# Kernel tuning notes

Hardware: AMD Instinct MI355X
Metric: run time of the kernel (lower is better)

## Reference

```python
import jax, jax.numpy as jnp
import numpy as np


def setup_inputs() -> dict:
    key = jax.random.key(0)
    k1, k2, k3, k4, k5 = jax.random.split(key, 5)
    b, c, k, h, w = 8, 512, 19, 128, 128
    x = jax.random.normal(k1, (b, c, h, w), dtype=jnp.float32)
    # mask_conv: 1x1 conv ichn->ochn (weight [k, c], bias [k])
    Wm = jax.random.normal(k2, (k, c), dtype=jnp.float32) * (1.0 / np.sqrt(c))
    bm = jax.random.normal(k3, (k,), dtype=jnp.float32) * 0.02
    # filter_conv: grouped 1x1 conv, groups=k -> per-class [c_out, c_in] matmul
    Wf = jax.random.normal(k4, (k, c, c), dtype=jnp.float32) * (1.0 / np.sqrt(c))
    bf = jax.random.normal(k5, (k, c), dtype=jnp.float32) * 0.02
    return {"x": x, "Wm": Wm, "bm": bm, "Wf": Wf, "bf": bf}


def reference(x, Wm, bm, Wf, bf):
    b, c, h, w = x.shape
    k = Wm.shape[0]
    # mask_conv (1x1) + sigmoid -> [b, k, h, w]
    pre_mask = jnp.einsum('bchw,kc->bkhw', x, Wm) + bm[None, :, None, None]
    mask = jax.nn.sigmoid(pre_mask)
    # masked pooling: bmm(mask [b,k,hw], feat [b,hw,c]) / (h*w) -> [b, k, c]
    class_feat = jnp.einsum('bkhw,bchw->bkc', mask, x) / (h * w)
    # grouped 1x1 filter_conv: per class k, [c_out, c_in] GEMM on class_feat
    filters = jnp.einsum('koc,bkc->bko', Wf, class_feat) + bf[None, :, :]  # [b, k, c]
    # per-sample dynamic 1x1 conv (groups=b) == batched GEMM over channels
    pred = jnp.einsum('bkc,bchw->bkhw', filters, x)
    return pred
```

## Files before the change

### kernel.cpp

```cpp
#include <hip/hip_runtime.h>
#include <math.h>

#define BB 8
#define CC 512
#define KK 19
#define HWHW 16384
#define INV_HW (1.0f/16384.0f)

typedef __attribute__((ext_vector_type(8))) short bf16x8;
typedef __attribute__((ext_vector_type(4))) short s16x4;
typedef __attribute__((ext_vector_type(4))) float f32x4;

__device__ __forceinline__ unsigned short f2bf(float f) {
    unsigned int u = __float_as_uint(f);
    u = (u + 0x7fffu + ((u >> 16) & 1u)) >> 16;
    return (unsigned short)u;
}

__device__ __forceinline__ unsigned int pk_bf16(float a, float b) {
    unsigned int r;
    asm("v_cvt_pk_bf16_f32 %0, %1, %2" : "=v"(r) : "v"(a), "v"(b));
    return r;
}

__global__ __launch_bounds__(256, 3) void k_s1(const float* __restrict__ x,
                                               const float* __restrict__ Wm,
                                               const float* __restrict__ bm,
                                               unsigned short* __restrict__ mask) {
    __shared__ short wm[20 * CC];
    __shared__ short xt[2][128 * 64];
    const int tid = threadIdx.x;
    const int b = blockIdx.x >> 7;
    const int p0 = (blockIdx.x & 127) << 7;
    const float* xb = x + ((size_t)b * CC) * HWHW + p0;

    for (int u = tid; u < 20 * 128; u += 256) {
        const int k = u >> 7;
        const int c4 = (u & 127) << 2;
        float4 w = {0.f, 0.f, 0.f, 0.f};
        if (k < KK) w = *(const float4*)(Wm + k * CC + c4);
        s16x4 v = { (short)f2bf(w.x), (short)f2bf(w.y), (short)f2bf(w.z), (short)f2bf(w.w) };
        *(s16x4*)&wm[(k << 9) + (((c4 >> 3) ^ (k & 7)) << 3) + (c4 & 7)] = v;
    }

    const int wv = tid >> 6, ln = tid & 63;
    const int lm = ln & 15, q = ln >> 4;
    const f32x4 zz = {0.f, 0.f, 0.f, 0.f};
    f32x4 acc[2][2];
    acc[0][0] = zz; acc[0][1] = zz; acc[1][0] = zz; acc[1][1] = zz;

    const int cg0 = tid >> 5;
    const int pA  = (tid & 31) << 2;
    const float* sA = xb + (size_t)(cg0 << 2) * HWHW + pA;
    const float* sB = xb + (size_t)((cg0 + 8) << 2) * HWHW + pA;

    float4 Fa[8], Fb[8];
#pragma unroll
    for (int j = 0; j < 4; ++j) {
        Fa[j]     = *(const float4*)(sA + (size_t)j * HWHW);
        Fa[4 + j] = *(const float4*)(sB + (size_t)j * HWHW);
    }

#pragma unroll
    for (int cs = 0; cs < 8; ++cs) {
        const float4* cur = (cs & 1) ? Fb : Fa;
        float4* nxt = (cs & 1) ? Fa : Fb;
        if (cs < 7) {
            const size_t co = (size_t)((cs + 1) << 6) * HWHW;
#pragma unroll
            for (int j = 0; j < 4; ++j) {
                nxt[j]     = *(const float4*)(sA + co + (size_t)j * HWHW);
                nxt[4 + j] = *(const float4*)(sB + co + (size_t)j * HWHW);
            }
        }
        short* xts = (short*)xt[cs & 1];
#pragma unroll
        for (int h = 0; h < 2; ++h) {
            const int cg = cg0 + (h << 3);
            const float* G0 = (const float*)&cur[(h << 2) + 0];
            const float* G1 = (const float*)&cur[(h << 2) + 1];
            const float* G2 = (const float*)&cur[(h << 2) + 2];
            const float* G3 = (const float*)&cur[(h << 2) + 3];
#pragma unroll
            for (int j = 0; j < 4; ++j) {
                const int pr = pA + j;
                uint2 v = make_uint2(pk_bf16(G0[j], G1[j]), pk_bf16(G2[j], G3[j]));
                *(uint2*)&xts[(pr << 6) + (((cg >> 1) ^ (pr & 7)) << 3) + ((cg & 1) << 2)] = v;
            }
        }
        asm volatile("s_waitcnt lgkmcnt(0)" ::: "memory");
        __builtin_amdgcn_s_barrier();
        asm volatile("" ::: "memory");
#pragma unroll
        for (int ks = 0; ks < 2; ++ks) {
            const int gch = (cs << 3) + (ks << 2) + q;
            const int m1 = (lm < 3) ? (16 + lm) : 19;
            bf16x8 a0 = *(const bf16x8*)&wm[(lm << 9) + ((gch ^ (lm & 7)) << 3)];
            bf16x8 a1 = *(const bf16x8*)&wm[(m1 << 9) + ((gch ^ (m1 & 7)) << 3)];
            const int lch = (ks << 2) + q;
#pragma unroll
            for (int nt = 0; nt < 2; ++nt) {
                const int pr = (((wv << 1) + nt) << 4) + lm;
                bf16x8 bv = *(const bf16x8*)&xts[(pr << 6) + ((lch ^ (pr & 7)) << 3)];
                acc[0][nt] = __builtin_amdgcn_mfma_f32_16x16x32_bf16(a0, bv, acc[0][nt], 0, 0, 0);
                acc[1][nt] = __builtin_amdgcn_mfma_f32_16x16x32_bf16(a1, bv, acc[1][nt], 0, 0, 0);
            }
        }
    }

    unsigned short* mb = mask + ((size_t)b * KK) * HWHW + p0;
#pragma unroll
    for (int mt = 0; mt < 2; ++mt)
#pragma unroll
        for (int r = 0; r < 4; ++r) {
            const int k = (mt << 4) + (q << 2) + r;
            if (k < KK) {
                const float bias = bm[k];
#pragma unroll
                for (int nt = 0; nt < 2; ++nt) {
                    const int p = (((wv << 1) + nt) << 4) + lm;
                    const float t = acc[mt][nt][r] + bias;
                    mb[(size_t)k * HWHW + p] = f2bf(1.0f / (1.0f + __expf(-t)));
                }
            }
        }
}

__global__ __launch_bounds__(256, 4) void k_s2(const float* __restrict__ x,
                                               const unsigned short* __restrict__ mask,
                                               float* __restrict__ cf_part) {
    __shared__ short mt_[2][20 * 64];
    __shared__ short xtl[2][64 * 64];
    const int tid = threadIdx.x;
    const int s = blockIdx.x & 15;
    const int ct = (blockIdx.x >> 4) & 7;
    const int b = blockIdx.x >> 7;
    const int wv = tid >> 6, ln = tid & 63;
    const int lm = ln & 15, q = ln >> 4;
    const float* xb = x + ((size_t)b * CC + (ct << 6)) * HWHW + (s << 10);
    const unsigned short* mbs = mask + ((size_t)b * KK) * HWHW + (s << 10);

    const int mk = tid >> 3, mch = tid & 7;
    const int xc = tid >> 4;
    const int pq = tid & 15;

    const f32x4 zz = {0.f, 0.f, 0.f, 0.f};
    f32x4 acc[2];
    acc[0] = zz; acc[1] = zz;

    float4 Xa[4], Xb[4];
    uint4 Ma = make_uint4(0u,0u,0u,0u), Mb = make_uint4(0u,0u,0u,0u);

    if (tid < 160 && mk < KK) Ma = *(const uint4*)(mbs + (size_t)mk * HWHW + (mch << 3));
#pragma unroll
    for (int r = 0; r < 4; ++r)
        Xa[r] = *(const float4*)(xb + (size_t)(xc + (r << 4)) * HWHW + (pq << 2));

#pragma unroll
    for (int kp = 0; kp < 16; ++kp) {
        const float4* curX = (kp & 1) ? Xb : Xa;
        float4* nxtX = (kp & 1) ? Xa : Xb;
        const uint4 curM = (kp & 1) ? Mb : Ma;
        uint4* nxtM = (kp & 1) ? &Ma : &Mb;
        if (kp < 15) {
            if (tid < 160 && mk < KK)
                *nxtM = *(const uint4*)(mbs + (size_t)mk * HWHW + ((kp + 1) << 6) + (mch << 3));
#pragma unroll
            for (int r = 0; r < 4; ++r)
                nxtX[r] = *(const float4*)(xb + (size_t)(xc + (r << 4)) * HWHW + ((kp + 1) << 6) + (pq << 2));
        }
        short* mts = (short*)mt_[kp & 1];
        short* xls = (short*)xtl[kp & 1];
        if (tid < 160)
            *(uint4*)&mts[(mk << 6) + ((mch ^ (mk & 7)) << 3)] = curM;
#pragma unroll
        for (int r = 0; r < 4; ++r) {
            const int c = xc + (r << 4);
            const float* G = (const float*)&curX[r];
            uint2 v = make_uint2(pk_bf16(G[0], G[1]), pk_bf16(G[2], G[3]));
            *(uint2*)&xls[(c << 6) + (((pq >> 1) ^ (c & 7)) << 3) + ((pq & 1) << 2)] = v;
        }
        asm volatile("s_waitcnt lgkmcnt(0)" ::: "memory");
        __builtin_amdgcn_s_barrier();
        asm volatile("" ::: "memory");
#pragma unroll
        for (int ks = 0; ks < 2; ++ks) {
            const int pch = (ks << 2) + q;
            const int cr = (wv << 4) + lm;
            bf16x8 bv = *(const bf16x8*)&xls[(cr << 6) + ((pch ^ (cr & 7)) << 3)];
            const int m1 = (lm < 3) ? (16 + lm) : 19;
            bf16x8 a0 = *(const bf16x8*)&mts[(lm << 6) + ((pch ^ (lm & 7)) << 3)];
            bf16x8 a1 = *(const bf16x8*)&mts[(m1 << 6) + ((pch ^ (m1 & 7)) << 3)];
            acc[0] = __builtin_amdgcn_mfma_f32_16x16x32_bf16(a0, bv, acc[0], 0, 0, 0);
            acc[1] = __builtin_amdgcn_mfma_f32_16x16x32_bf16(a1, bv, acc[1], 0, 0, 0);
        }
    }

    float* dst = cf_part + ((size_t)(s * BB + b) * KK) * CC + (ct << 6) + (wv << 4) + lm;
#pragma unroll
    for (int mt = 0; mt < 2; ++mt)
#pragma unroll
        for (int r = 0; r < 4; ++r) {
            const int k = (mt << 4) + (q << 2) + r;
            if (k < KK) dst[(size_t)k * CC] = acc[mt][r];
        }
}

__global__ __launch_bounds__(256) void k_s2r(const float* __restrict__ part,
                                             float* __restrict__ cf) {
    const int i = blockIdx.x * 256 + threadIdx.x;
    if (i >= BB * KK * CC) return;
    const int b = i / (KK * CC);
    const int rem = i - b * (KK * CC);
    float sum = 0.0f;
#pragma unroll
    for (int s = 0; s < 16; ++s)
        sum += part[((size_t)(s * BB + b) * KK) * CC + rem];
    cf[i] = sum * INV_HW;
}

__global__ __launch_bounds__(256) void k_filters(const float* __restrict__ Wf,
                                                 const float* __restrict__ bf,
                                                 const float* __restrict__ cf,
                                                 float* __restrict__ fil) {
    const int blk = blockIdx.x;
    const int k = blk >> 7;
    const int o = ((blk & 127) << 2) + (threadIdx.x >> 6);
    const int lane = threadIdx.x & 63;
    const float* wrow = Wf + ((size_t)k * CC + o) * CC;

    float acc[BB];
#pragma unroll
    for (int b = 0; b < BB; ++b) acc[b] = 0.0f;
#pragma unroll
    for (int j = 0; j < CC / 64; ++j) {
        const int c = lane + (j << 6);
        const float wv = wrow[c];
#pragma unroll
        for (int b = 0; b < BB; ++b)
            acc[b] += wv * cf[((size_t)b * KK + k) * CC + c];
    }
#pragma unroll
    for (int b = 0; b < BB; ++b) {
#pragma unroll
        for (int off = 32; off > 0; off >>= 1)
            acc[b] += __shfl_down(acc[b], off, 64);
    }
    if (lane == 0) {
        const float bias = bf[k * CC + o];
#pragma unroll
        for (int b = 0; b < BB; ++b)
            fil[((size_t)b * KK + k) * CC + o] = acc[b] + bias;
    }
}

__global__ __launch_bounds__(256, 3) void k_s4(const float* __restrict__ x,
                                               const float* __restrict__ fil,
                                               float* __restrict__ out) {
    __shared__ short wm[20 * CC];
    __shared__ short xt[2][128 * 64];
    const int tid = threadIdx.x;
    const int b = blockIdx.x >> 7;
    const int p0 = (blockIdx.x & 127) << 7;
    const float* xb = x + ((size_t)b * CC) * HWHW + p0;
    const float* fb = fil + ((size_t)b * KK) * CC;

    for (int u = tid; u < 20 * 128; u += 256) {
        const int k = u >> 7;
        const int c4 = (u & 127) << 2;
        float4 w = {0.f, 0.f, 0.f, 0.f};
        if (k < KK) w = *(const float4*)(fb + k * CC + c4);
        s16x4 v = { (short)f2bf(w.x), (short)f2bf(w.y), (short)f2bf(w.z), (short)f2bf(w.w) };
        *(s16x4*)&wm[(k << 9) + (((c4 >> 3) ^ (k & 7)) << 3) + (c4 & 7)] = v;
    }

    const int wv = tid >> 6, ln = tid & 63;
    const int lm = ln & 15, q = ln >> 4;
    const f32x4 zz = {0.f, 0.f, 0.f, 0.f};
    f32x4 acc[2][2];
    acc[0][0] = zz; acc[0][1] = zz; acc[1][0] = zz; acc[1][1] = zz;

    const int cg0 = tid >> 5;
    const int pA  = (tid & 31) << 2;
    const float* sA = xb + (size_t)(cg0 << 2) * HWHW + pA;
    const float* sB = xb + (size_t)((cg0 + 8) << 2) * HWHW + pA;

    float4 Fa[8], Fb[8];
#pragma unroll
    for (int j = 0; j < 4; ++j) {
        Fa[j]     = *(const float4*)(sA + (size_t)j * HWHW);
        Fa[4 + j] = *(const float4*)(sB + (size_t)j * HWHW);
    }

#pragma unroll
    for (int cs = 0; cs < 8; ++cs) {
        const float4* cur = (cs & 1) ? Fb : Fa;
        float4* nxt = (cs & 1) ? Fa : Fb;
        if (cs < 7) {
            const size_t co = (size_t)((cs + 1) << 6) * HWHW;
#pragma unroll
            for (int j = 0; j < 4; ++j) {
                nxt[j]     = *(const float4*)(sA + co + (size_t)j * HWHW);
                nxt[4 + j] = *(const float4*)(sB + co + (size_t)j * HWHW);
            }
        }
        short* xts = (short*)xt[cs & 1];
#pragma unroll
        for (int h = 0; h < 2; ++h) {
            const int cg = cg0 + (h << 3);
            const float* G0 = (const float*)&cur[(h << 2) + 0];
            const float* G1 = (const float*)&cur[(h << 2) + 1];
            const float* G2 = (const float*)&cur[(h << 2) + 2];
            const float* G3 = (const float*)&cur[(h << 2) + 3];
#pragma unroll
            for (int j = 0; j < 4; ++j) {
                const int pr = pA + j;
                uint2 v = make_uint2(pk_bf16(G0[j], G1[j]), pk_bf16(G2[j], G3[j]));
                *(uint2*)&xts[(pr << 6) + (((cg >> 1) ^ (pr & 7)) << 3) + ((cg & 1) << 2)] = v;
            }
        }
        asm volatile("s_waitcnt lgkmcnt(0)" ::: "memory");
        __builtin_amdgcn_s_barrier();
        asm volatile("" ::: "memory");
#pragma unroll
        for (int ks = 0; ks < 2; ++ks) {
            const int gch = (cs << 3) + (ks << 2) + q;
            const int m1 = (lm < 3) ? (16 + lm) : 19;
            bf16x8 a0 = *(const bf16x8*)&wm[(lm << 9) + ((gch ^ (lm & 7)) << 3)];
            bf16x8 a1 = *(const bf16x8*)&wm[(m1 << 9) + ((gch ^ (m1 & 7)) << 3)];
            const int lch = (ks << 2) + q;
#pragma unroll
            for (int nt = 0; nt < 2; ++nt) {
                const int pr = (((wv << 1) + nt) << 4) + lm;
                bf16x8 bv = *(const bf16x8*)&xts[(pr << 6) + ((lch ^ (pr & 7)) << 3)];
                acc[0][nt] = __builtin_amdgcn_mfma_f32_16x16x32_bf16(a0, bv, acc[0][nt], 0, 0, 0);
                acc[1][nt] = __builtin_amdgcn_mfma_f32_16x16x32_bf16(a1, bv, acc[1][nt], 0, 0, 0);
            }
        }
    }

    float* ob = out + ((size_t)b * KK) * HWHW + p0;
#pragma unroll
    for (int mt = 0; mt < 2; ++mt)
#pragma unroll
        for (int r = 0; r < 4; ++r) {
            const int k = (mt << 4) + (q << 2) + r;
            if (k < KK) {
#pragma unroll
                for (int nt = 0; nt < 2; ++nt) {
                    const int p = (((wv << 1) + nt) << 4) + lm;
                    ob[(size_t)k * HWHW + p] = acc[mt][nt][r];
                }
            }
        }
}

extern "C" void kernel_launch(void* const* d_in, const int* in_sizes, int n_in,
                              void* d_out, int out_size, void* d_ws, size_t ws_size,
                              hipStream_t stream) {
    const float* x  = (const float*)d_in[0];
    const float* Wm = (const float*)d_in[1];
    const float* bm = (const float*)d_in[2];
    const float* Wf = (const float*)d_in[3];
    const float* bf = (const float*)d_in[4];
    float* out = (float*)d_out;

    unsigned short* mask = (unsigned short*)d_ws;
    float* cf_part = (float*)((char*)d_ws + (size_t)BB * KK * HWHW * 2);
    float* cf  = cf_part + (size_t)16 * BB * KK * CC;
    float* fil = cf + (size_t)BB * KK * CC;

    k_s1<<<1024, 256, 0, stream>>>(x, Wm, bm, mask);
    k_s2<<<1024, 256, 0, stream>>>(x, mask, cf_part);
    k_s2r<<<(BB * KK * CC + 255) / 256, 256, 0, stream>>>(cf_part, cf);
    k_filters<<<KK * 128, 256, 0, stream>>>(Wf, bf, cf, fil);
    k_s4<<<1024, 256, 0, stream>>>(x, fil, out);
}
```

Baseline: 470.3 us.

## Stage pre-swizzled bf16 copies of x in the first pass for reuse downstream

```diff
diff --git a/kernel.cpp b/kernel.cpp
--- a/kernel.cpp
+++ b/kernel.cpp
@@ -26,12 +26,15 @@
 __global__ __launch_bounds__(256, 3) void k_s1(const float* __restrict__ x,
                                                const float* __restrict__ Wm,
                                                const float* __restrict__ bm,
-                                               unsigned short* __restrict__ mask) {
+                                               unsigned short* __restrict__ mask,
+                                               unsigned short* __restrict__ xt4g,
+                                               unsigned short* __restrict__ xt2g) {
     __shared__ short wm[20 * CC];
     __shared__ short xt[2][128 * 64];
     const int tid = threadIdx.x;
     const int b = blockIdx.x >> 7;
-    const int p0 = (blockIdx.x & 127) << 7;
+    const int pt = blockIdx.x & 127;
+    const int p0 = pt << 7;
     const float* xb = x + ((size_t)b * CC) * HWHW + p0;
 
     for (int u = tid; u < 20 * 128; u += 256) {
@@ -51,8 +54,14 @@
 
     const int cg0 = tid >> 5;
     const int pA  = (tid & 31) << 2;
+    const int pqT = (tid & 31) & 15;
+    const int sS  = pt >> 3;
+    const int kpT = ((pt & 7) << 1) | ((tid & 31) >> 4);
     const float* sA = xb + (size_t)(cg0 << 2) * HWHW + pA;
     const float* sB = xb + (size_t)((cg0 + 8) << 2) * HWHW + pA;
+    unsigned short* t4fix = xt4g + ((size_t)((b << 7) | pt) << 16);
+    unsigned short* t2fix = xt2g + ((size_t)(b << 3) << 20)
+                                 + ((size_t)((sS << 4) | kpT) << 12);
 
     float4 Fa[8], Fb[8];
 #pragma unroll
@@ -74,6 +83,8 @@
             }
         }
         short* xts = (short*)xt[cs & 1];
+        unsigned short* t4 = t4fix + ((size_t)cs << 13);
+        unsigned short* t2 = t2fix + ((size_t)cs << 20);
 #pragma unroll
         for (int h = 0; h < 2; ++h) {
             const int cg = cg0 + (h << 3);
@@ -85,7 +96,17 @@
             for (int j = 0; j < 4; ++j) {
                 const int pr = pA + j;
                 uint2 v = make_uint2(pk_bf16(G0[j], G1[j]), pk_bf16(G2[j], G3[j]));
-                *(uint2*)&xts[(pr << 6) + (((cg >> 1) ^ (pr & 7)) << 3) + ((cg & 1) << 2)] = v;
+                const int idx = (pr << 6) + (((cg >> 1) ^ (pr & 7)) << 3) + ((cg & 1) << 2);
+                *(uint2*)&xts[idx] = v;
+                *(uint2*)&t4[idx] = v;
+            }
+#pragma unroll
+            for (int rr = 0; rr < 4; ++rr) {
+                const int cl = (cg << 2) + rr;
+                const float* Gr = (const float*)&cur[(h << 2) + rr];
+                uint2 w = make_uint2(pk_bf16(Gr[0], Gr[1]), pk_bf16(Gr[2], Gr[3]));
+                const int idx2 = (cl << 6) + (((pqT >> 1) ^ (cl & 7)) << 3) + ((pqT & 1) << 2);
+                *(uint2*)&t2[idx2] = w;
             }
         }
         asm volatile("s_waitcnt lgkmcnt(0)" ::: "memory");
@@ -126,7 +147,7 @@
         }
 }
 
-__global__ __launch_bounds__(256, 4) void k_s2(const float* __restrict__ x,
+__global__ __launch_bounds__(256, 4) void k_s2(const unsigned short* __restrict__ xt2g,
                                                const unsigned short* __restrict__ mask,
                                                float* __restrict__ cf_part) {
     __shared__ short mt_[2][20 * 64];
@@ -137,49 +158,40 @@
     const int b = blockIdx.x >> 7;
     const int wv = tid >> 6, ln = tid & 63;
     const int lm = ln & 15, q = ln >> 4;
-    const float* xb = x + ((size_t)b * CC + (ct << 6)) * HWHW + (s << 10);
     const unsigned short* mbs = mask + ((size_t)b * KK) * HWHW + (s << 10);
+    const unsigned short* tb = xt2g + ((size_t)((((b << 3) | ct) << 4) | s) << 16);
 
     const int mk = tid >> 3, mch = tid & 7;
-    const int xc = tid >> 4;
-    const int pq = tid & 15;
 
     const f32x4 zz = {0.f, 0.f, 0.f, 0.f};
     f32x4 acc[2];
     acc[0] = zz; acc[1] = zz;
 
-    float4 Xa[4], Xb[4];
+    uint4 Xa[2], Xb2[2];
     uint4 Ma = make_uint4(0u,0u,0u,0u), Mb = make_uint4(0u,0u,0u,0u);
 
     if (tid < 160 && mk < KK) Ma = *(const uint4*)(mbs + (size_t)mk * HWHW + (mch << 3));
-#pragma unroll
-    for (int r = 0; r < 4; ++r)
-        Xa[r] = *(const float4*)(xb + (size_t)(xc + (r << 4)) * HWHW + (pq << 2));
+    Xa[0] = *(const uint4*)(tb + (tid << 4));
+    Xa[1] = *(const uint4*)(tb + (tid << 4) + 8);
 
 #pragma unroll
     for (int kp = 0; kp < 16; ++kp) {
-        const float4* curX = (kp & 1) ? Xb : Xa;
-        float4* nxtX = (kp & 1) ? Xa : Xb;
+        const uint4* curX = (kp & 1) ? Xb2 : Xa;
+        uint4* nxtX = (kp & 1) ? Xa : Xb2;
         const uint4 curM = (kp & 1) ? Mb : Ma;
         uint4* nxtM = (kp & 1) ? &Ma : &Mb;
         if (kp < 15) {
             if (tid < 160 && mk < KK)
                 *nxtM = *(const uint4*)(mbs + (size_t)mk * HWHW + ((kp + 1) << 6) + (mch << 3));
-#pragma unroll
-            for (int r = 0; r < 4; ++r)
-                nxtX[r] = *(const float4*)(xb + (size_t)(xc + (r << 4)) * HWHW + ((kp + 1) << 6) + (pq << 2));
+            nxtX[0] = *(const uint4*)(tb + ((kp + 1) << 12) + (tid << 4));
+            nxtX[1] = *(const uint4*)(tb + ((kp + 1) << 12) + (tid << 4) + 8);
         }
         short* mts = (short*)mt_[kp & 1];
         short* xls = (short*)xtl[kp & 1];
         if (tid < 160)
             *(uint4*)&mts[(mk << 6) + ((mch ^ (mk & 7)) << 3)] = curM;
-#pragma unroll
-        for (int r = 0; r < 4; ++r) {
-            const int c = xc + (r << 4);
-            const float* G = (const float*)&curX[r];
-            uint2 v = make_uint2(pk_bf16(G[0], G[1]), pk_bf16(G[2], G[3]));
-            *(uint2*)&xls[(c << 6) + (((pq >> 1) ^ (c & 7)) << 3) + ((pq & 1) << 2)] = v;
-        }
+        *(uint4*)&xls[(tid << 4)] = curX[0];
+        *(uint4*)&xls[(tid << 4) + 8] = curX[1];
         asm volatile("s_waitcnt lgkmcnt(0)" ::: "memory");
         __builtin_amdgcn_s_barrier();
         asm volatile("" ::: "memory");
@@ -254,16 +266,17 @@
     }
 }
 
-__global__ __launch_bounds__(256, 3) void k_s4(const float* __restrict__ x,
+__global__ __launch_bounds__(256, 3) void k_s4(const unsigned short* __restrict__ xt4g,
                                                const float* __restrict__ fil,
                                                float* __restrict__ out) {
     __shared__ short wm[20 * CC];
     __shared__ short xt[2][128 * 64];
     const int tid = threadIdx.x;
     const int b = blockIdx.x >> 7;
-    const int p0 = (blockIdx.x & 127) << 7;
-    const float* xb = x + ((size_t)b * CC) * HWHW + p0;
+    const int pt = blockIdx.x & 127;
+    const int p0 = pt << 7;
     const float* fb = fil + ((size_t)b * KK) * CC;
+    const unsigned short* tb = xt4g + ((size_t)((b << 7) | pt) << 16);
 
     for (int u = tid; u < 20 * 128; u += 256) {
         const int k = u >> 7;
@@ -280,45 +293,24 @@
     f32x4 acc[2][2];
     acc[0][0] = zz; acc[0][1] = zz; acc[1][0] = zz; acc[1][1] = zz;
 
-    const int cg0 = tid >> 5;
-    const int pA  = (tid & 31) << 2;
-    const float* sA = xb + (size_t)(cg0 << 2) * HWHW + pA;
-    const float* sB = xb + (size_t)((cg0 + 8) << 2) * HWHW + pA;
-
-    float4 Fa[8], Fb[8];
-#pragma unroll
-    for (int j = 0; j < 4; ++j) {
-        Fa[j]     = *(const float4*)(sA + (size_t)j * HWHW);
-        Fa[4 + j] = *(const float4*)(sB + (size_t)j * HWHW);
-    }
+    uint4 Ta[4], Tb4[4];
+#pragma unroll
+    for (int r = 0; r < 4; ++r)
+        Ta[r] = *(const uint4*)(tb + (tid << 5) + (r << 3));
 
 #pragma unroll
     for (int cs = 0; cs < 8; ++cs) {
-        const float4* cur = (cs & 1) ? Fb : Fa;
-        float4* nxt = (cs & 1) ? Fa : Fb;
+        const uint4* cur = (cs & 1) ? Tb4 : Ta;
+        uint4* nxt = (cs & 1) ? Ta : Tb4;
         if (cs < 7) {
-            const size_t co = (size_t)((cs + 1) << 6) * HWHW;
-#pragma unroll
-            for (int j = 0; j < 4; ++j) {
-                nxt[j]     = *(const float4*)(sA + co + (size_t)j * HWHW);
-                nxt[4 + j] = *(const float4*)(sB + co + (size_t)j * HWHW);
-            }
+#pragma unroll
+            for (int r = 0; r < 4; ++r)
+                nxt[r] = *(const uint4*)(tb + ((cs + 1) << 13) + (tid << 5) + (r << 3));
         }
         short* xts = (short*)xt[cs & 1];
 #pragma unroll
-        for (int h = 0; h < 2; ++h) {
-            const int cg = cg0 + (h << 3);
-            const float* G0 = (const float*)&cur[(h << 2) + 0];
-            const float* G1 = (const float*)&cur[(h << 2) + 1];
-            const float* G2 = (const float*)&cur[(h << 2) + 2];
-            const float* G3 = (const float*)&cur[(h << 2) + 3];
-#pragma unroll
-            for (int j = 0; j < 4; ++j) {
-                const int pr = pA + j;
-                uint2 v = make_uint2(pk_bf16(G0[j], G1[j]), pk_bf16(G2[j], G3[j]));
-                *(uint2*)&xts[(pr << 6) + (((cg >> 1) ^ (pr & 7)) << 3) + ((cg & 1) << 2)] = v;
-            }
-        }
+        for (int r = 0; r < 4; ++r)
+            *(uint4*)&xts[(tid << 5) + (r << 3)] = cur[r];
         asm volatile("s_waitcnt lgkmcnt(0)" ::: "memory");
         __builtin_amdgcn_s_barrier();
         asm volatile("" ::: "memory");
@@ -365,14 +357,17 @@
     const float* bf = (const float*)d_in[4];
     float* out = (float*)d_out;
 
-    unsigned short* mask = (unsigned short*)d_ws;
-    float* cf_part = (float*)((char*)d_ws + (size_t)BB * KK * HWHW * 2);
-    float* cf  = cf_part + (size_t)16 * BB * KK * CC;
-    float* fil = cf + (size_t)BB * KK * CC;
-
-    k_s1<<<1024, 256, 0, stream>>>(x, Wm, bm, mask);
-    k_s2<<<1024, 256, 0, stream>>>(x, mask, cf_part);
+    char* p = (char*)d_ws;
+    unsigned short* mask = (unsigned short*)p;  p += (size_t)BB * KK * HWHW * 2;
+    float* cf_part = (float*)p;                 p += (size_t)16 * BB * KK * CC * 4;
+    float* cf  = (float*)p;                     p += (size_t)BB * KK * CC * 4;
+    float* fil = (float*)p;                     p += (size_t)BB * KK * CC * 4;
+    unsigned short* xt4g = (unsigned short*)p;  p += (size_t)BB * 128 * 8 * 16384;
+    unsigned short* xt2g = (unsigned short*)p;
+
+    k_s1<<<1024, 256, 0, stream>>>(x, Wm, bm, mask, xt4g, xt2g);
+    k_s2<<<1024, 256, 0, stream>>>(xt2g, mask, cf_part);
     k_s2r<<<(BB * KK * CC + 255) / 256, 256, 0, stream>>>(cf_part, cf);
     k_filters<<<KK * 128, 256, 0, stream>>>(Wf, bf, cf, fil);
-    k_s4<<<1024, 256, 0, stream>>>(x, fil, out);
-}
+    k_s4<<<1024, 256, 0, stream>>>(xt4g, fil, out);
+}
```

New measurement: 505.6 us. 7.5% more time.
